# Optimization experiments

Hardware: AMD Instinct MI355X
Metric: run time of the kernel (lower is better)

The kernel has to match this reference:

```python
import jax, jax.numpy as jnp
import numpy as np

FORGET_BIAS = 1.0
LAYERS = 2


def setup_inputs() -> dict:
    key = jax.random.key(0)
    ks = jax.random.split(key, 10)
    B, T, H, V = 64, 50, 256, 50000
    G = 4 * H
    s = 1.0 / np.sqrt(H)
    return {
        "input_data": jax.random.randint(ks[0], (B, T), 0, V, dtype=jnp.int64),
        "embedding": jax.random.uniform(ks[1], (V, H), jnp.float32, -1.0, 1.0),
        "Wx": jax.random.normal(ks[2], (LAYERS, H, G), jnp.float32) * s,
        "Uh": jax.random.normal(ks[3], (LAYERS, H, G), jnp.float32) * s,
        "alpha": jax.random.uniform(ks[4], (LAYERS, G), jnp.float32),
        "beta1": jax.random.uniform(ks[5], (LAYERS, G), jnp.float32),
        "beta2": jax.random.uniform(ks[6], (LAYERS, G), jnp.float32),
        "bias": jnp.zeros((LAYERS, G), jnp.float32),
        "softmax_w": jax.random.normal(ks[7], (V, H), jnp.float32) * s,
        "softmax_b": jnp.full((V,), 0.1, jnp.float32),
    }


def _mi_lstm_stack(inputs_tbh, Wx, Uh, alpha, beta1, beta2, bias):
    # inputs_tbh: [T, B, H]; params have leading layer axis [L, ...]
    T, B, H = inputs_tbh.shape
    c0 = jnp.zeros((LAYERS, B, H), inputs_tbh.dtype)
    h0 = jnp.zeros((LAYERS, B, H), inputs_tbh.dtype)

    def step(carry, x_t):
        c, h = carry
        inp = x_t
        new_c, new_h = [], []
        for l in range(LAYERS):
            xh = inp @ Wx[l]          # [B, 4H]
            hh = h[l] @ Uh[l]         # [B, 4H]
            gates = alpha[l] * xh * hh + beta1[l] * xh + beta2[l] * hh + bias[l]
            i, j, f, o = jnp.split(gates, 4, axis=-1)
            c_l = c[l] * jax.nn.sigmoid(f + FORGET_BIAS) + jax.nn.sigmoid(i) * jnp.tanh(j)
            h_l = jnp.tanh(c_l) * jax.nn.sigmoid(o)
            new_c.append(c_l)
            new_h.append(h_l)
            inp = h_l
        return (jnp.stack(new_c), jnp.stack(new_h)), inp

    (_, _), outs = jax.lax.scan(step, (c0, h0), inputs_tbh)
    return outs  # [T, B, H] top-layer hidden states


def reference(input_data, embedding, Wx, Uh, alpha, beta1, beta2, bias, softmax_w, softmax_b):
    # embedding lookup: [B, T, H] -> time-major [T, B, H]
    x = embedding[input_data]
    outs = _mi_lstm_stack(jnp.transpose(x, (1, 0, 2)), Wx, Uh, alpha, beta1, beta2, bias)
    # batch-major flatten like tf.reshape(outputs, [-1, rnn_size]) on [B, T, H]
    H = outs.shape[-1]
    flat = jnp.transpose(outs, (1, 0, 2)).reshape(-1, H)  # [B*T, H]
    logits = flat @ softmax_w.T + softmax_b               # [B*T, V]
    return logits
```

## Files before the change

kernel.cpp:

```cpp
#include <hip/hip_runtime.h>
#include <hip/hip_bf16.h>
#include <math.h>

#define B_ 64
#define T_ 50
#define H_ 256
#define G_ 1024
#define V_ 50000
#define NBLK 32
#define BSTRIDE 64

using f16x8 = __attribute__((ext_vector_type(8))) _Float16;
using f16x4 = __attribute__((ext_vector_type(4))) _Float16;
using f32x4 = __attribute__((ext_vector_type(4))) float;

__device__ __forceinline__ float sigm(float x) { return 1.0f / (1.0f + expf(-x)); }

__global__ __launch_bounds__(64) void embed_k(const int* __restrict__ idx,
                                              const float* __restrict__ emb,
                                              _Float16* __restrict__ x16)
{
    const int row = blockIdx.x;
    const int b = row & (B_ - 1);
    const int t = row >> 6;
    const int id = idx[b * T_ + t];
    const float4 v = *reinterpret_cast<const float4*>(emb + (size_t)id * H_ + threadIdx.x * 4);
    f16x4 h;
    h[0] = (_Float16)v.x; h[1] = (_Float16)v.y;
    h[2] = (_Float16)v.z; h[3] = (_Float16)v.w;
    *reinterpret_cast<f16x4*>(x16 + (size_t)row * H_ + threadIdx.x * 4) = h;
}

__global__ __launch_bounds__(256) void conv_half(const float* __restrict__ in,
                                                 _Float16* __restrict__ out, int n)
{
    const int i = (blockIdx.x * 256 + threadIdx.x) * 8;
    if (i + 8 <= n) {
        const float4 v0 = *reinterpret_cast<const float4*>(in + i);
        const float4 v1 = *reinterpret_cast<const float4*>(in + i + 4);
        f16x8 h;
        h[0] = (_Float16)v0.x; h[1] = (_Float16)v0.y;
        h[2] = (_Float16)v0.z; h[3] = (_Float16)v0.w;
        h[4] = (_Float16)v1.x; h[5] = (_Float16)v1.y;
        h[6] = (_Float16)v1.z; h[7] = (_Float16)v1.w;
        *reinterpret_cast<f16x8*>(out + i) = h;
    }
}

__global__ __launch_bounds__(256) void pack_wx0(const float* __restrict__ Wx0,
                                                _Float16* __restrict__ wxT)
{
    __shared__ _Float16 ts[64][65];
    const int k0 = blockIdx.x * 64;
    const int n0 = blockIdx.y * 64;
    const int tr = threadIdx.x >> 6;
    const int tc = threadIdx.x & 63;
#pragma unroll
    for (int i = 0; i < 16; ++i) {
        const int r = i * 4 + tr;
        ts[r][tc] = (_Float16)Wx0[(size_t)(k0 + r) * G_ + n0 + tc];
    }
    __syncthreads();
#pragma unroll
    for (int i = 0; i < 16; ++i) {
        const int c = i * 4 + tr;
        wxT[(size_t)(n0 + c) * H_ + k0 + tc] = ts[tc][c];
    }
}

__global__ __launch_bounds__(256) void pack_w_rec(const float* __restrict__ Uh0,
                                                  const float* __restrict__ Wx1,
                                                  const float* __restrict__ Uh1,
                                                  _Float16* __restrict__ wpk)
{
    const int c = blockIdx.x;
    const int m = blockIdx.y;
    const float* __restrict__ src = (m == 0) ? Uh0 : (m == 1) ? Wx1 : Uh1;
    _Float16* __restrict__ dst = wpk + (((size_t)c * 3 + m) << 13);
    for (int i = threadIdx.x; i < 8192; i += 256) {
        const int k = i >> 5;
        const int col = i & 31;
        const int colg = ((col >> 3) << 8) + (c << 3) + (col & 7);
        dst[(col << 8) + k] = (_Float16)src[(size_t)k * G_ + colg];
    }
}

__device__ __forceinline__ void gload_lds16(const void* g, void* l)
{
    __builtin_amdgcn_global_load_lds(
        (const __attribute__((address_space(1))) unsigned int*)g,
        (__attribute__((address_space(3))) unsigned int*)l, 16, 0, 0);
}

__device__ __forceinline__ void gbar_arrive(int* slot)
{
    __syncthreads();
    if (threadIdx.x == 0) {
        __threadfence();
        __hip_atomic_fetch_add(slot, 1, __ATOMIC_RELAXED, __HIP_MEMORY_SCOPE_AGENT);
    }
}

__device__ __forceinline__ void gbar_wait_fast(int* slot)
{
    if (threadIdx.x == 0) {
        while (__hip_atomic_load(slot, __ATOMIC_RELAXED, __HIP_MEMORY_SCOPE_AGENT) < NBLK)
            __builtin_amdgcn_s_sleep(1);
    }
    __syncthreads();
    __threadfence();
}

#define PM 128
#define PN 128
#define PK 64

__global__ __launch_bounds__(256) void gemm16_mfma(
    const _Float16* __restrict__ A16,
    const _Float16* __restrict__ B16,
    float* __restrict__ C)
{
    __shared__ __align__(16) _Float16 Asub[PM * PK];
    __shared__ __align__(16) _Float16 Bsub[PN * PK];

    const int tid = threadIdx.x;
    const int l = tid & 63;
    const int w = tid >> 6;
    const int wm = w >> 1, wn = w & 1;

    const int n0 = blockIdx.x * PN;
    const int m0 = blockIdx.y * PM;

    f32x4 acc[4][4] = {};

    for (int k0 = 0; k0 < H_; k0 += PK) {
#pragma unroll
        for (int is = 0; is < 4; ++is) {
            const int i = is * 256 + tid;
            const int r = i >> 3;
            const int ch = (i & 7) ^ (r & 7);
            gload_lds16(A16 + (size_t)(m0 + r) * H_ + k0 + ch * 8, &Asub[i * 8]);
            gload_lds16(B16 + (size_t)(n0 + r) * H_ + k0 + ch * 8, &Bsub[i * 8]);
        }
        __syncthreads();

#pragma unroll
        for (int ks = 0; ks < 2; ++ks) {
            f16x8 af[4], bf[4];
#pragma unroll
            for (int i = 0; i < 4; ++i) {
                const int r = wm * 64 + i * 16 + (l & 15);
                const int ch = (ks * 4 + (l >> 4)) ^ (r & 7);
                af[i] = *reinterpret_cast<const f16x8*>(&Asub[r * PK + ch * 8]);
            }
#pragma unroll
            for (int jf = 0; jf < 4; ++jf) {
                const int r = wn * 64 + jf * 16 + (l & 15);
                const int ch = (ks * 4 + (l >> 4)) ^ (r & 7);
                bf[jf] = *reinterpret_cast<const f16x8*>(&Bsub[r * PK + ch * 8]);
            }
#pragma unroll
            for (int i = 0; i < 4; ++i)
#pragma unroll
                for (int jf = 0; jf < 4; ++jf)
                    acc[i][jf] = __builtin_amdgcn_mfma_f32_16x16x32_f16(
                        af[i], bf[jf], acc[i][jf], 0, 0, 0);
        }
        __syncthreads();
    }

    const int rb = (l >> 4) << 2;
    const int cl = l & 15;
#pragma unroll
    for (int jf = 0; jf < 4; ++jf) {
        const int col = n0 + wn * 64 + jf * 16 + cl;
#pragma unroll
        for (int i = 0; i < 4; ++i) {
            const int rowb = m0 + wm * 64 + i * 16 + rb;
#pragma unroll
            for (int r = 0; r < 4; ++r)
                C[(size_t)(rowb + r) * G_ + col] = acc[i][jf][r];
        }
    }
}

__global__ __launch_bounds__(256) void mi_rec(
    const _Float16* __restrict__ wpk,
    const float* __restrict__ xh0,
    _Float16* __restrict__ h0x,
    _Float16* __restrict__ h1x,
    _Float16* __restrict__ outsH,
    int* __restrict__ bars,
    const float* __restrict__ alpha, const float* __restrict__ b1,
    const float* __restrict__ b2, const float* __restrict__ bsv)
{
    __shared__ __align__(16) _Float16 h0l[16384];
    __shared__ __align__(16) _Float16 h1l[16384];
    __shared__ __align__(16) _Float16 wl[24576];
    __shared__ float gA[2112], gB[2112];
    __shared__ float c0l[512], c1l[512];

    const int c = blockIdx.x;
    const int tid = threadIdx.x;
    const int l = tid & 63;
    const int w = tid >> 6;

    for (int i = tid; i < 2048; i += 256) {
        *reinterpret_cast<f16x8*>(&h0l[i << 3]) = f16x8{};
        *reinterpret_cast<f16x8*>(&h1l[i << 3]) = f16x8{};
    }
    for (int i = tid; i < 512; i += 256) { c0l[i] = 0.f; c1l[i] = 0.f; }

    for (int i = tid; i < 3072; i += 256) {
        const int m = i >> 10;
        const int col = (i >> 5) & 31;
        const int ch = i & 31;
        const f16x8 v = *reinterpret_cast<const f16x8*>(
            &wpk[(((size_t)c * 3 + m) * 32 + col) * 256 + (ch << 3)]);
        *reinterpret_cast<f16x8*>(
            &wl[(m * 32 + col) * 256 + ((ch ^ (col & 7)) << 3)]) = v;
    }

    const int u = tid & 7, b0 = tid >> 3;
    const int jl = (c << 3) + u;
    float al0[4], b10[4], b20[4], bs0[4], al1[4], b11[4], b21[4], bs1[4];
#pragma unroll
    for (int g = 0; g < 4; ++g) {
        const int col = (g << 8) + jl;
        al0[g] = alpha[col];        b10[g] = b1[col];
        b20[g] = b2[col];           bs0[g] = bsv[col];
        al1[g] = alpha[G_ + col];   b11[g] = b1[G_ + col];
        b21[g] = b2[G_ + col];      bs1[g] = bsv[G_ + col];
    }
    __syncthreads();

    const int arow = (w << 4) + (l & 15);
    const int cA = l & 15, cB = 16 + (l & 15);
    const int kq = l >> 4;

    auto MM = [&](const _Float16* am, const _Float16* bm, f32x4& A0, f32x4& A1) {
#pragma unroll
        for (int s = 0; s < 8; ++s) {
            const int ck = (s << 2) + kq;
            const f16x8 af = *reinterpret_cast<const f16x8*>(
                &am[(arow << 8) + ((ck ^ (arow & 7)) << 3)]);
            const f16x8 bf0 = *reinterpret_cast<const f16x8*>(
                &bm[(cA << 8) + ((ck ^ (cA & 7)) << 3)]);
            const f16x8 bf1 = *reinterpret_cast<const f16x8*>(
                &bm[(cB << 8) + ((ck ^ (cB & 7)) << 3)]);
            A0 = __builtin_amdgcn_mfma_f32_16x16x32_f16(af, bf0, A0, 0, 0, 0);
            A1 = __builtin_amdgcn_mfma_f32_16x16x32_f16(af, bf1, A1, 0, 0, 0);
        }
    };
    auto STG = [&](float* gl, f32x4 A0, f32x4 A1) {
        const int rb = (w << 4) + (kq << 2);
#pragma unroll
        for (int r = 0; r < 4; ++r) {
            gl[(rb + r) * 33 + cA] = A0[r];
            gl[(rb + r) * 33 + cB] = A1[r];
        }
    };
    auto STAGE_H = [&](const _Float16* src, _Float16* dst) {
#pragma unroll
        for (int it = 0; it < 8; ++it) {
            const int idx = (it << 8) + tid;
            const int row = idx >> 5, ch = idx & 31;
            const f16x8 v = *reinterpret_cast<const f16x8*>(&src[(row << 8) + (ch << 3)]);
            *reinterpret_cast<f16x8*>(&dst[(row << 8) + ((ch ^ (row & 7)) << 3)]) = v;
        }
    };

    for (int s = 0; s <= T_; ++s) {
        const int p = s & 1;
        _Float16* h0w = h0x + (p << 14);
        _Float16* h1w = h1x + (p << 14);

        if (s < T_) {
            float xv[2][4];
#pragma unroll
            for (int bb = 0; bb < 2; ++bb)
#pragma unroll
                for (int g = 0; g < 4; ++g)
                    xv[bb][g] = xh0[(((size_t)(s * B_ + (b0 + (bb << 5)))) << 10)
                                    + (g << 8) + jl];

            f32x4 A0 = {}, A1 = {};
            MM(h0l, wl, A0, A1);
            STG(gA, A0, A1);
            __syncthreads();
#pragma unroll
            for (int bb = 0; bb < 2; ++bb) {
                const int b = b0 + (bb << 5);
                float g4[4];
#pragma unroll
                for (int g = 0; g < 4; ++g) {
                    const float a = gA[b * 33 + (g << 3) + u];
                    const float x = xv[bb][g];
                    g4[g] = al0[g] * x * a + b10[g] * x + b20[g] * a + bs0[g];
                }
                const float cn = c0l[(b << 3) + u] * sigm(g4[2] + 1.f)
                               + sigm(g4[0]) * tanhf(g4[1]);
                c0l[(b << 3) + u] = cn;
                h0w[(b << 8) + jl] = (_Float16)(tanhf(cn) * sigm(g4[3]));
            }
            __syncthreads();
        }

        if (s > 0) {
            f32x4 X0 = {}, X1 = {}, H0 = {}, H1 = {};
            MM(h0l, wl + 1 * 8192, X0, X1);
            MM(h1l, wl + 2 * 8192, H0, H1);
            STG(gA, X0, X1);
            STG(gB, H0, H1);
            __syncthreads();
#pragma unroll
            for (int bb = 0; bb < 2; ++bb) {
                const int b = b0 + (bb << 5);
                float g4[4];
#pragma unroll
                for (int g = 0; g < 4; ++g) {
                    const float xa = gA[b * 33 + (g << 3) + u];
                    const float ha = gB[b * 33 + (g << 3) + u];
                    g4[g] = al1[g] * xa * ha + b11[g] * xa + b21[g] * ha + bs1[g];
                }
                const float cn = c1l[(b << 3) + u] * sigm(g4[2] + 1.f)
                               + sigm(g4[0]) * tanhf(g4[1]);
                c1l[(b << 3) + u] = cn;
                const float hn = tanhf(cn) * sigm(g4[3]);
                h1w[(b << 8) + jl] = (_Float16)hn;
                outsH[(((size_t)b * T_ + (s - 1)) << 8) + jl] = (_Float16)hn;
            }
        }

        if (s < T_) {
            gbar_arrive(bars + s * BSTRIDE);
            gbar_wait_fast(bars + s * BSTRIDE);
            STAGE_H(h0w, h0l);
            if (s > 0) STAGE_H(h1w, h1l);
            __syncthreads();
        }
    }
}

__global__ __launch_bounds__(256) void proj_mfma(
    const _Float16* __restrict__ A16,
    const _Float16* __restrict__ B16,
    const float* __restrict__ bias,
    float* __restrict__ C)
{
    __shared__ __align__(16) char smem[33792];
    _Float16* Asub = (_Float16*)smem;
    _Float16* Bsub = (_Float16*)(smem + 16384);
    float*    tbuf = (float*)smem;

    const int tid = threadIdx.x;
    const int l = tid & 63;
    const int w = tid >> 6;
    const int wm = w >> 1, wn = w & 1;

    const int n0 = blockIdx.x * PN;
    const int m0 = blockIdx.y * PM;

    f32x4 acc[4][4] = {};

    for (int k0 = 0; k0 < H_; k0 += PK) {
#pragma unroll
        for (int is = 0; is < 4; ++is) {
            const int i = is * 256 + tid;
            const int r = i >> 3;
            const int ch = (i & 7) ^ (r & 7);
            gload_lds16(A16 + (size_t)(m0 + r) * H_ + k0 + ch * 8, &Asub[i * 8]);
            int n = n0 + r; if (n > V_ - 1) n = V_ - 1;
            gload_lds16(B16 + (size_t)n * H_ + k0 + ch * 8, &Bsub[i * 8]);
        }
        __syncthreads();

#pragma unroll
        for (int ks = 0; ks < 2; ++ks) {
            f16x8 af[4], bf[4];
#pragma unroll
            for (int i = 0; i < 4; ++i) {
                const int r = wm * 64 + i * 16 + (l & 15);
                const int ch = (ks * 4 + (l >> 4)) ^ (r & 7);
                af[i] = *reinterpret_cast<const f16x8*>(&Asub[r * PK + ch * 8]);
            }
#pragma unroll
            for (int jf = 0; jf < 4; ++jf) {
                const int r = wn * 64 + jf * 16 + (l & 15);
                const int ch = (ks * 4 + (l >> 4)) ^ (r & 7);
                bf[jf] = *reinterpret_cast<const f16x8*>(&Bsub[r * PK + ch * 8]);
            }
#pragma unroll
            for (int i = 0; i < 4; ++i)
#pragma unroll
                for (int jf = 0; jf < 4; ++jf)
                    acc[i][jf] = __builtin_amdgcn_mfma_f32_16x16x32_f16(
                        af[i], bf[jf], acc[i][jf], 0, 0, 0);
        }
        __syncthreads();
    }

    const int rbl = (l >> 4) << 2;
    const int cll = l & 15;
#pragma unroll
    for (int ph = 0; ph < 2; ++ph) {
        if (ph) __syncthreads();
        if (wm == ph) {
#pragma unroll
            for (int jf = 0; jf < 4; ++jf)
#pragma unroll
                for (int i = 0; i < 4; ++i)
#pragma unroll
                    for (int r = 0; r < 4; ++r)
                        tbuf[(i * 16 + rbl + r) * 132 + wn * 64 + jf * 16 + cll]
                            = acc[i][jf][r];
        }
        __syncthreads();
#pragma unroll
        for (int k = 0; k < 8; ++k) {
            const int f = k * 256 + tid;
            const int lr = f >> 5;
            const int c4 = (f & 31) << 2;
            const int col = n0 + c4;
            if (col < V_) {
                float4 v = *reinterpret_cast<const float4*>(&tbuf[lr * 132 + c4]);
                const float4 bv = *reinterpret_cast<const float4*>(&bias[col]);
                v.x += bv.x; v.y += bv.y; v.z += bv.z; v.w += bv.w;
                *reinterpret_cast<float4*>(
                    &C[(size_t)(m0 + ph * 64 + lr) * V_ + col]) = v;
            }
        }
    }
}

extern "C" void kernel_launch(void* const* d_in, const int* in_sizes, int n_in,
                              void* d_out, int out_size, void* d_ws, size_t ws_size,
                              hipStream_t stream)
{
    const int*   idx   = (const int*)  d_in[0];
    const float* emb   = (const float*)d_in[1];
    const float* Wx    = (const float*)d_in[2];
    const float* Uh    = (const float*)d_in[3];
    const float* alpha = (const float*)d_in[4];
    const float* b1    = (const float*)d_in[5];
    const float* b2    = (const float*)d_in[6];
    const float* bsv   = (const float*)d_in[7];
    const float* sw    = (const float*)d_in[8];
    const float* sb    = (const float*)d_in[9];
    float* out = (float*)d_out;

    char* wsb = (char*)d_ws;
    _Float16* x16   = (_Float16*)(wsb);
    float*    xh0   = (float*)   (wsb + 1638400);
    _Float16* outsH = (_Float16*)(wsb + 14745600);
    _Float16* w16   = (_Float16*)(wsb + 16384000);
    _Float16* wxT   = (_Float16*)(wsb + 41984000);
    _Float16* wpk   = (_Float16*)(wsb + 42508288);
    _Float16* h0x   = (_Float16*)(wsb + 44081152);
    _Float16* h1x   = (_Float16*)(wsb + 44146688);
    int*      bars  = (int*)     (wsb + 44212224);

    const float* Wx0 = Wx;
    const float* Wx1 = Wx + (size_t)H_ * G_;
    const float* Uh0 = Uh;
    const float* Uh1 = Uh + (size_t)H_ * G_;

    (void)hipMemsetAsync(bars, 0, 16384, stream);

    {
        dim3 grid(NBLK, 3);
        pack_w_rec<<<grid, 256, 0, stream>>>(Uh0, Wx1, Uh1, wpk);
    }
    {
        dim3 grid(4, 16);
        pack_wx0<<<grid, 256, 0, stream>>>(Wx0, wxT);
    }
    conv_half<<<(V_ * H_) / 2048, 256, 0, stream>>>(sw, w16, V_ * H_);

    embed_k<<<T_ * B_, 64, 0, stream>>>(idx, emb, x16);

    {
        dim3 grid(G_ / PN, 3200 / PM);
        gemm16_mfma<<<grid, 256, 0, stream>>>(x16, wxT, xh0);
    }

    mi_rec<<<NBLK, 256, 0, stream>>>(wpk, xh0, h0x, h1x, outsH, bars,
                                     alpha, b1, b2, bsv);

    {
        dim3 grid((V_ + PN - 1) / PN, 3200 / PM);
        proj_mfma<<<grid, 256, 0, stream>>>(outsH, w16, sb, out);
    }
}
```

Baseline: 677.8 us.

## Fuse prep kernels, store xh0 in fp16, unpad projection staging buffer

Merges the weight-packing, Wx0 transpose and embedding gather kernels into one launch of 960 blocks, removing two kernel launches. The precomputed input-gate products xh0 are now written and read as fp16 instead of fp32, which halves the traffic the recurrent kernel reads each step. The projection's LDS staging stride drops from 132 to 128 floats to shrink shared memory, which may bring LDS bank conflicts back and lowers gate-input precision.

```diff
diff --git a/kernel.cpp b/kernel.cpp
--- a/kernel.cpp
+++ b/kernel.cpp
@@ -16,19 +16,62 @@
 
 __device__ __forceinline__ float sigm(float x) { return 1.0f / (1.0f + expf(-x)); }
 
-__global__ __launch_bounds__(64) void embed_k(const int* __restrict__ idx,
+__global__ __launch_bounds__(256) void prep_k(const int* __restrict__ idx,
                                               const float* __restrict__ emb,
+                                              const float* __restrict__ Uh0,
+                                              const float* __restrict__ Wx1,
+                                              const float* __restrict__ Uh1,
+                                              const float* __restrict__ Wx0,
+                                              _Float16* __restrict__ wpk,
+                                              _Float16* __restrict__ wxT,
                                               _Float16* __restrict__ x16)
 {
-    const int row = blockIdx.x;
-    const int b = row & (B_ - 1);
-    const int t = row >> 6;
-    const int id = idx[b * T_ + t];
-    const float4 v = *reinterpret_cast<const float4*>(emb + (size_t)id * H_ + threadIdx.x * 4);
-    f16x4 h;
-    h[0] = (_Float16)v.x; h[1] = (_Float16)v.y;
-    h[2] = (_Float16)v.z; h[3] = (_Float16)v.w;
-    *reinterpret_cast<f16x4*>(x16 + (size_t)row * H_ + threadIdx.x * 4) = h;
+    __shared__ _Float16 ts[64][65];
+    const int bid = blockIdx.x;
+    const int tid = threadIdx.x;
+
+    if (bid < 96) {
+        const int c = bid & 31;
+        const int m = bid >> 5;
+        const float* __restrict__ src = (m == 0) ? Uh0 : (m == 1) ? Wx1 : Uh1;
+        _Float16* __restrict__ dst = wpk + (((size_t)c * 3 + m) << 13);
+        for (int i = tid; i < 8192; i += 256) {
+            const int k = i >> 5;
+            const int col = i & 31;
+            const int colg = ((col >> 3) << 8) + (c << 3) + (col & 7);
+            dst[(col << 8) + k] = (_Float16)src[(size_t)k * G_ + colg];
+        }
+    } else if (bid < 160) {
+        const int r2 = bid - 96;
+        const int k0 = (r2 & 3) * 64;
+        const int n0 = (r2 >> 2) * 64;
+        const int tr = tid >> 6;
+        const int tc = tid & 63;
+#pragma unroll
+        for (int i = 0; i < 16; ++i) {
+            const int r = i * 4 + tr;
+            ts[r][tc] = (_Float16)Wx0[(size_t)(k0 + r) * G_ + n0 + tc];
+        }
+        __syncthreads();
+#pragma unroll
+        for (int i = 0; i < 16; ++i) {
+            const int c = i * 4 + tr;
+            wxT[(size_t)(n0 + c) * H_ + k0 + tc] = ts[tc][c];
+        }
+    } else {
+        const int task = (bid - 160) * 256 + tid;
+        const int row = task >> 6;
+        const int ch = task & 63;
+        const int b = row & (B_ - 1);
+        const int t = row >> 6;
+        const int id = idx[b * T_ + t];
+        const float4 v = *reinterpret_cast<const float4*>(
+            emb + (size_t)id * H_ + ch * 4);
+        f16x4 h;
+        h[0] = (_Float16)v.x; h[1] = (_Float16)v.y;
+        h[2] = (_Float16)v.z; h[3] = (_Float16)v.w;
+        *reinterpret_cast<f16x4*>(x16 + (size_t)row * H_ + ch * 4) = h;
+    }
 }
 
 __global__ __launch_bounds__(256) void conv_half(const float* __restrict__ in,
@@ -47,44 +90,6 @@
     }
 }
 
-__global__ __launch_bounds__(256) void pack_wx0(const float* __restrict__ Wx0,
-                                                _Float16* __restrict__ wxT)
-{
-    __shared__ _Float16 ts[64][65];
-    const int k0 = blockIdx.x * 64;
-    const int n0 = blockIdx.y * 64;
-    const int tr = threadIdx.x >> 6;
-    const int tc = threadIdx.x & 63;
-#pragma unroll
-    for (int i = 0; i < 16; ++i) {
-        const int r = i * 4 + tr;
-        ts[r][tc] = (_Float16)Wx0[(size_t)(k0 + r) * G_ + n0 + tc];
-    }
-    __syncthreads();
-#pragma unroll
-    for (int i = 0; i < 16; ++i) {
-        const int c = i * 4 + tr;
-        wxT[(size_t)(n0 + c) * H_ + k0 + tc] = ts[tc][c];
-    }
-}
-
-__global__ __launch_bounds__(256) void pack_w_rec(const float* __restrict__ Uh0,
-                                                  const float* __restrict__ Wx1,
-                                                  const float* __restrict__ Uh1,
-                                                  _Float16* __restrict__ wpk)
-{
-    const int c = blockIdx.x;
-    const int m = blockIdx.y;
-    const float* __restrict__ src = (m == 0) ? Uh0 : (m == 1) ? Wx1 : Uh1;
-    _Float16* __restrict__ dst = wpk + (((size_t)c * 3 + m) << 13);
-    for (int i = threadIdx.x; i < 8192; i += 256) {
-        const int k = i >> 5;
-        const int col = i & 31;
-        const int colg = ((col >> 3) << 8) + (c << 3) + (col & 7);
-        dst[(col << 8) + k] = (_Float16)src[(size_t)k * G_ + colg];
-    }
-}
-
 __device__ __forceinline__ void gload_lds16(const void* g, void* l)
 {
     __builtin_amdgcn_global_load_lds(
@@ -118,7 +123,7 @@
 __global__ __launch_bounds__(256) void gemm16_mfma(
     const _Float16* __restrict__ A16,
     const _Float16* __restrict__ B16,
-    float* __restrict__ C)
+    _Float16* __restrict__ C)
 {
     __shared__ __align__(16) _Float16 Asub[PM * PK];
     __shared__ __align__(16) _Float16 Bsub[PN * PK];
@@ -179,14 +184,14 @@
             const int rowb = m0 + wm * 64 + i * 16 + rb;
 #pragma unroll
             for (int r = 0; r < 4; ++r)
-                C[(size_t)(rowb + r) * G_ + col] = acc[i][jf][r];
+                C[(size_t)(rowb + r) * G_ + col] = (_Float16)acc[i][jf][r];
         }
     }
 }
 
 __global__ __launch_bounds__(256) void mi_rec(
     const _Float16* __restrict__ wpk,
-    const float* __restrict__ xh0,
+    const _Float16* __restrict__ xh0h,
     _Float16* __restrict__ h0x,
     _Float16* __restrict__ h1x,
     _Float16* __restrict__ outsH,
@@ -281,8 +286,8 @@
             for (int bb = 0; bb < 2; ++bb)
 #pragma unroll
                 for (int g = 0; g < 4; ++g)
-                    xv[bb][g] = xh0[(((size_t)(s * B_ + (b0 + (bb << 5)))) << 10)
-                                    + (g << 8) + jl];
+                    xv[bb][g] = (float)xh0h[(((size_t)(s * B_ + (b0 + (bb << 5)))) << 10)
+                                            + (g << 8) + jl];
 
             f32x4 A0 = {}, A1 = {};
             MM(h0l, wl, A0, A1);
@@ -348,7 +353,7 @@
     const float* __restrict__ bias,
     float* __restrict__ C)
 {
-    __shared__ __align__(16) char smem[33792];
+    __shared__ __align__(16) char smem[32768];
     _Float16* Asub = (_Float16*)smem;
     _Float16* Bsub = (_Float16*)(smem + 16384);
     float*    tbuf = (float*)smem;
@@ -412,7 +417,7 @@
                 for (int i = 0; i < 4; ++i)
 #pragma unroll
                     for (int r = 0; r < 4; ++r)
-                        tbuf[(i * 16 + rbl + r) * 132 + wn * 64 + jf * 16 + cll]
+                        tbuf[(i * 16 + rbl + r) * 128 + wn * 64 + jf * 16 + cll]
                             = acc[i][jf][r];
         }
         __syncthreads();
@@ -423,7 +428,7 @@
             const int c4 = (f & 31) << 2;
             const int col = n0 + c4;
             if (col < V_) {
-                float4 v = *reinterpret_cast<const float4*>(&tbuf[lr * 132 + c4]);
+                float4 v = *reinterpret_cast<const float4*>(&tbuf[lr * 128 + c4]);
                 const float4 bv = *reinterpret_cast<const float4*>(&bias[col]);
                 v.x += bv.x; v.y += bv.y; v.z += bv.z; v.w += bv.w;
                 *reinterpret_cast<float4*>(
@@ -451,7 +456,7 @@
 
     char* wsb = (char*)d_ws;
     _Float16* x16   = (_Float16*)(wsb);
-    float*    xh0   = (float*)   (wsb + 1638400);
+    _Float16* xh0h  = (_Float16*)(wsb + 1638400);
     _Float16* outsH = (_Float16*)(wsb + 14745600);
     _Float16* w16   = (_Float16*)(wsb + 16384000);
     _Float16* wxT   = (_Float16*)(wsb + 41984000);
@@ -467,24 +472,16 @@
 
     (void)hipMemsetAsync(bars, 0, 16384, stream);
 
-    {
-        dim3 grid(NBLK, 3);
-        pack_w_rec<<<grid, 256, 0, stream>>>(Uh0, Wx1, Uh1, wpk);
-    }
-    {
-        dim3 grid(4, 16);
-        pack_wx0<<<grid, 256, 0, stream>>>(Wx0, wxT);
-    }
+    prep_k<<<960, 256, 0, stream>>>(idx, emb, Uh0, Wx1, Uh1, Wx0, wpk, wxT, x16);
+
     conv_half<<<(V_ * H_) / 2048, 256, 0, stream>>>(sw, w16, V_ * H_);
-
-    embed_k<<<T_ * B_, 64, 0, stream>>>(idx, emb, x16);
 
     {
         dim3 grid(G_ / PN, 3200 / PM);
-        gemm16_mfma<<<grid, 256, 0, stream>>>(x16, wxT, xh0);
-    }
-
-    mi_rec<<<NBLK, 256, 0, stream>>>(wpk, xh0, h0x, h1x, outsH, bars,
+        gemm16_mfma<<<grid, 256, 0, stream>>>(x16, wxT, xh0h);
+    }
+
+    mi_rec<<<NBLK, 256, 0, stream>>>(wpk, xh0h, h0x, h1x, outsH, bars,
                                      alpha, b1, b2, bsv);
 
     {
```

Result: no change. 681.8 us (+0.6%).
